# Kernel optimization log

Hardware: AMD Instinct MI355X
Metric: run time of the kernel (lower is better)

## Reference

```python
import jax, jax.numpy as jnp
import numpy as np

COMMITMENT_LOSS_WEIGHT = 0.25


def setup_inputs() -> dict:
    key = jax.random.key(0)
    k1, k2 = jax.random.split(key)
    B, H, W, C = 64, 32, 32, 256
    D, K = H * W, 1024  # embedding_dim = H*W per the rearrange+reshape in call()
    x = jax.random.normal(k1, (B, H, W, C), dtype=jnp.float32)
    # Orthogonal initializer (like tf.keras.initializers.Orthogonal) via QR
    E = jnp.linalg.qr(jax.random.normal(k2, (D, K), dtype=jnp.float32))[0]
    return {"x": x, "embeddings": E.astype(jnp.float32)}


def reference(x, embeddings):
    B, H, W, C = x.shape
    D = H * W  # embedding_dim
    # einops: 'b h w c -> b c (h w)'
    cont = jnp.transpose(x, (0, 3, 1, 2)).reshape(B, C, D)
    flat = cont.reshape(-1, D)  # [B*C, D]
    # squared L2 distances via norm + matmul (as in get_discretised)
    dists = (jnp.sum(flat * flat, axis=1, keepdims=True)
             + jnp.sum(embeddings * embeddings, axis=0)
             - 2.0 * (flat @ embeddings))  # [B*C, K]
    idx = jnp.argmin(dists, axis=1)  # [B*C]
    # one_hot @ embeddings.T == direct gather of codebook columns
    quantised = embeddings.T[idx].reshape(B, C, D)
    codebook_loss = jnp.mean((jax.lax.stop_gradient(cont) - quantised) ** 2)
    commitment_loss = COMMITMENT_LOSS_WEIGHT * jnp.mean(
        (cont - jax.lax.stop_gradient(quantised)) ** 2)
    loss = codebook_loss + commitment_loss  # layer add_loss terms, summed
    # einops: 'b c (h w) -> b h w c'
    q_bhwc = jnp.transpose(quantised.reshape(B, C, H, W), (0, 2, 3, 1))
    discretised = idx.reshape(-1, C)  # [B, C]
    # straight-through estimator
    q_out = x + jax.lax.stop_gradient(q_bhwc - x)
    return q_out, discretised, loss
```

## Files before the change

### kernel.cpp

```cpp
#include <hip/hip_runtime.h>
#include <float.h>
#include <stdint.h>

#define B_   64
#define C_   256
#define D_   1024
#define K_   1024
#define M_   16384
#define NX_  16777216
#define DISC_OFF NX_
#define LOSS_OFF (NX_ + M_)

typedef _Float16 h8 __attribute__((ext_vector_type(8)));
typedef float    f4 __attribute__((ext_vector_type(4)));

#define XSCALE 512.0f
#define ESCALE 2048.0f
#define DOT_UNSCALE_2 (2.0f / 1048576.0f)

#define WS_EH  0
#define WS_EL  524288
#define WS_CN  1048576
#define WS_PCN 1049600
#define WS_PV  1180672
#define WS_PI  1246208

__device__ __forceinline__ void async16(const _Float16* g, _Float16* l) {
    __builtin_amdgcn_global_load_lds(
        (const __attribute__((address_space(1))) unsigned int*)g,
        (__attribute__((address_space(3))) unsigned int*)l, 16, 0, 0);
}

__global__ __launch_bounds__(256) void esplit_kernel(const float* __restrict__ E,
                                                     _Float16* __restrict__ Eh,
                                                     _Float16* __restrict__ El,
                                                     float* __restrict__ pcn) {
    const int t  = threadIdx.x;
    const int o  = blockIdx.x;
    const int d0 = o * 8;
    const int n0 = t * 4;
    float4 row[8];
    #pragma unroll
    for (int i = 0; i < 8; ++i)
        row[i] = *(const float4*)(E + (size_t)(d0 + i) * K_ + n0);
    float s0 = 0.f, s1 = 0.f, s2 = 0.f, s3 = 0.f;
    h8 hh[4], ll[4];
    #pragma unroll
    for (int i = 0; i < 8; ++i) {
        const float* rp = (const float*)&row[i];
        #pragma unroll
        for (int j = 0; j < 4; ++j) {
            const float v  = rp[j];
            const float vs = v * ESCALE;
            const _Float16 h = (_Float16)vs;
            hh[j][i] = h;
            ll[j][i] = (_Float16)(vs - (float)h);
        }
        s0 = fmaf(rp[0], rp[0], s0);
        s1 = fmaf(rp[1], rp[1], s1);
        s2 = fmaf(rp[2], rp[2], s2);
        s3 = fmaf(rp[3], rp[3], s3);
    }
    float4 sv; sv.x = s0; sv.y = s1; sv.z = s2; sv.w = s3;
    *(float4*)(pcn + o * K_ + n0) = sv;
    const int nt    = n0 >> 4;
    const int kt    = o >> 2;
    const int lane0 = (n0 & 15) + (o & 3) * 16;
    const size_t base = ((size_t)(nt * 32 + kt) * 64 + lane0) * 8;
    #pragma unroll
    for (int j = 0; j < 4; ++j) {
        *(h8*)(Eh + base + (size_t)j * 8) = hh[j];
        *(h8*)(El + base + (size_t)j * 8) = ll[j];
    }
}

__global__ __launch_bounds__(256) void colnorm2_kernel(const float* __restrict__ pcn,
                                                       float* __restrict__ cn,
                                                       float* __restrict__ loss_slot) {
    __shared__ float sp[4][64];
    const int t    = threadIdx.x;
    const int col  = blockIdx.x * 64 + (t & 63);
    const int part = t >> 6;
    float s = 0.f;
    #pragma unroll 8
    for (int i = 0; i < 32; ++i) s += pcn[(part * 32 + i) * K_ + col];
    sp[part][t & 63] = s;
    __syncthreads();
    if (t < 64) cn[col] = (sp[0][t] + sp[1][t]) + (sp[2][t] + sp[3][t]);
    if (blockIdx.x == 0 && t == 0) *loss_slot = 0.0f;
}

__global__ __launch_bounds__(512, 2) void gemm_argmin_kernel(
        const float* __restrict__ x,
        const _Float16* __restrict__ Eh, const _Float16* __restrict__ El,
        const float* __restrict__ cn,
        float* __restrict__ pV, int* __restrict__ pI) {
    extern __shared__ _Float16 smem[];
    _Float16* Ab0 = smem;
    _Float16* Ab1 = smem + 8192;
    _Float16* Bb0 = smem + 16384;
    _Float16* Bb1 = smem + 32768;
    float* cV = (float*)(smem + 49152);
    int*   cI = (int*)(cV + 512);

    const int t    = threadIdx.x;
    const int rt   = blockIdx.x >> 2;
    const int ct   = blockIdx.x & 3;
    const int wave = t >> 6, lane = t & 63;
    const int lo16 = lane & 15, hi4 = lane >> 4;
    const int mq   = (wave & 1) * 64;
    const int nq   = (wave >> 1) * 64;
    const int nt0  = ct * 16;
    const int n0g  = ct * 256;

    const _Float16* srcB[4];
    _Float16* dstB0[4];
    _Float16* dstB1[4];
    #pragma unroll
    for (int i = 0; i < 4; ++i) {
        const int id = wave * 4 + i;
        const int plane = id >> 4, nt = id & 15;
        srcB[i]  = (plane ? El : Eh) + ((size_t)(nt0 + nt) * 32) * 512 + lane * 8;
        dstB0[i] = Bb0 + (plane * 16 + nt) * 512 + lane * 8;
        dstB1[i] = Bb1 + (plane * 16 + nt) * 512 + lane * 8;
    }

    const int b    = rt >> 1;
    const int c0   = (rt & 1) * 128;
    const int cl   = t & 127;
    const int ko8  = t >> 7;
    const float* xbase = x + ((size_t)(b * 1024 + ko8 * 8)) * 256 + c0 + cl;
    const int mt    = cl >> 4;
    const int lane0 = (cl & 15) + ko8 * 16;
    _Float16* wA[2] = { Ab0 + mt * 512 + lane0 * 8,
                        Ab1 + mt * 512 + lane0 * 8 };

    float av[8];
    auto loadA = [&](int s) {
        #pragma unroll
        for (int j = 0; j < 8; ++j)
            av[j] = xbase[((size_t)(s * 32) + j) * 256];
    };
    auto writeA = [&](_Float16* w) {
        h8 hh, ll;
        #pragma unroll
        for (int j = 0; j < 8; ++j) {
            const float vs = av[j] * XSCALE;
            const _Float16 h = (_Float16)vs;
            hh[j] = h;
            ll[j] = (_Float16)(vs - (float)h);
        }
        *(h8*)w = hh;
        *(h8*)(w + 4096) = ll;
    };

    f4 acc[4][4];
    const f4 zero = {0.f, 0.f, 0.f, 0.f};
    #pragma unroll
    for (int i = 0; i < 4; ++i)
        #pragma unroll
        for (int j = 0; j < 4; ++j) acc[i][j] = zero;

    #pragma unroll
    for (int i = 0; i < 4; ++i) async16(srcB[i], dstB0[i]);
    loadA(0);
    writeA(wA[0]);

    for (int s = 0; s < 32; ++s) {
        const int cur = s & 1;
        __syncthreads();
        if (s + 1 < 32) {
            #pragma unroll
            for (int i = 0; i < 4; ++i)
                async16(srcB[i] + (size_t)(s + 1) * 512, cur ? dstB0[i] : dstB1[i]);
            loadA(s + 1);
        }
        const _Float16* Abuf = cur ? Ab1 : Ab0;
        const _Float16* Bbuf = cur ? Bb1 : Bb0;

        h8 Bf[2][4];
        #pragma unroll
        for (int tn = 0; tn < 4; ++tn) {
            const int tixn = (nq >> 4) + tn;
            Bf[0][tn] = *(const h8*)&Bbuf[tixn * 512 + lane * 8];
            Bf[1][tn] = *(const h8*)&Bbuf[(16 + tixn) * 512 + lane * 8];
        }
        #pragma unroll
        for (int tm = 0; tm < 4; ++tm) {
            const int tixm = (mq >> 4) + tm;
            const h8 Ah = *(const h8*)&Abuf[tixm * 512 + lane * 8];
            const h8 Al = *(const h8*)&Abuf[(8 + tixm) * 512 + lane * 8];
            #pragma unroll
            for (int tn = 0; tn < 4; ++tn) {
                acc[tm][tn] = __builtin_amdgcn_mfma_f32_16x16x32_f16(Ah, Bf[0][tn], acc[tm][tn], 0, 0, 0);
                acc[tm][tn] = __builtin_amdgcn_mfma_f32_16x16x32_f16(Ah, Bf[1][tn], acc[tm][tn], 0, 0, 0);
                acc[tm][tn] = __builtin_amdgcn_mfma_f32_16x16x32_f16(Al, Bf[0][tn], acc[tm][tn], 0, 0, 0);
            }
        }
        if (s + 1 < 32) writeA(cur ? wA[0] : wA[1]);
    }

    float cnv[4];
    #pragma unroll
    for (int tn = 0; tn < 4; ++tn) cnv[tn] = cn[n0g + nq + tn * 16 + lo16];

    #pragma unroll
    for (int tm = 0; tm < 4; ++tm) {
        #pragma unroll
        for (int r = 0; r < 4; ++r) {
            float bv = FLT_MAX;
            int   bi = 0;
            #pragma unroll
            for (int tn = 0; tn < 4; ++tn) {
                const float v = cnv[tn] - acc[tm][tn][r] * DOT_UNSCALE_2;
                if (v < bv) { bv = v; bi = nq + tn * 16 + lo16; }
            }
            #pragma unroll
            for (int msk = 1; msk < 16; msk <<= 1) {
                const float ov = __shfl_xor(bv, msk, 64);
                const int   oi = __shfl_xor(bi, msk, 64);
                if (ov < bv || (ov == bv && oi < bi)) { bv = ov; bi = oi; }
            }
            if (lo16 == 0) {
                const int row = mq + tm * 16 + hi4 * 4 + r;
                const int g   = wave >> 1;
                cV[row * 4 + g] = bv;
                cI[row * 4 + g] = bi;
            }
        }
    }
    __syncthreads();
    if (t < 128) {
        float bv = FLT_MAX;
        int   bi = 0;
        #pragma unroll
        for (int g = 0; g < 4; ++g) {
            const float v = cV[t * 4 + g];
            const int   i = cI[t * 4 + g];
            if (v < bv || (v == bv && i < bi)) { bv = v; bi = i; }
        }
        const int row = rt * 128 + t;
        pV[row * 4 + ct] = bv;
        pI[row * 4 + ct] = n0g + bi;
    }
}

__global__ __launch_bounds__(256) void reduce_kernel(const float* __restrict__ pV,
                                                     const int* __restrict__ pI,
                                                     float* __restrict__ disc) {
    const int rid = blockIdx.x * 256 + threadIdx.x;
    float bv = FLT_MAX;
    int   bi = 0;
    #pragma unroll
    for (int c = 0; c < 4; ++c) {
        const float v = pV[rid * 4 + c];
        const int   i = pI[rid * 4 + c];
        if (v < bv || (v == bv && i < bi)) { bv = v; bi = i; }
    }
    disc[rid] = (float)bi;
}

__global__ __launch_bounds__(256) void finalize_kernel(const float* __restrict__ x,
                                                       const float* __restrict__ E,
                                                       const float* __restrict__ discf,
                                                       float* __restrict__ out,
                                                       float* __restrict__ loss) {
    __shared__ float Erow[1024];
    const int t = threadIdx.x;
    const int d = blockIdx.x;
    *(float4*)&Erow[t * 4] = *(const float4*)(E + (size_t)d * K_ + t * 4);
    __syncthreads();

    const int bl = t >> 6;
    const int c4 = (t & 63) * 4;
    float lsum = 0.f;
    #pragma unroll 4
    for (int bg = 0; bg < 64; bg += 4) {
        const int b = bg + bl;
        const float4 id4 = *(const float4*)(discf + b * 256 + c4);
        const size_t xoff = ((size_t)(b * 1024 + d) << 8) + c4;
        const float4 xv = *(const float4*)(x + xoff);
        const float e0 = Erow[(int)id4.x];
        const float e1 = Erow[(int)id4.y];
        const float e2 = Erow[(int)id4.z];
        const float e3 = Erow[(int)id4.w];
        float4 qv;
        qv.x = xv.x + (e0 - xv.x);
        qv.y = xv.y + (e1 - xv.y);
        qv.z = xv.z + (e2 - xv.z);
        qv.w = xv.w + (e3 - xv.w);
        *(float4*)(out + xoff) = qv;
        const float d0 = xv.x - e0, d1 = xv.y - e1, d2 = xv.z - e2, d3 = xv.w - e3;
        lsum += fmaf(d0, d0, fmaf(d1, d1, fmaf(d2, d2, d3 * d3)));
    }

    #pragma unroll
    for (int off = 32; off > 0; off >>= 1)
        lsum += __shfl_down(lsum, off);
    __shared__ float wsum[4];
    if ((t & 63) == 0) wsum[t >> 6] = lsum;
    __syncthreads();
    if (t == 0) {
        const float s = (wsum[0] + wsum[1]) + (wsum[2] + wsum[3]);
        atomicAdd(loss, s * (1.25f / 16777216.0f));
    }
}

extern "C" void kernel_launch(void* const* d_in, const int* in_sizes, int n_in,
                              void* d_out, int out_size, void* d_ws, size_t ws_size,
                              hipStream_t stream) {
    (void)in_sizes; (void)n_in; (void)out_size; (void)ws_size;
    const float* x = (const float*)d_in[0];
    const float* E = (const float*)d_in[1];
    float* out = (float*)d_out;
    float* ws  = (float*)d_ws;

    _Float16* Eh = (_Float16*)(ws + WS_EH);
    _Float16* El = (_Float16*)(ws + WS_EL);
    float* cn    = ws + WS_CN;
    float* pcn   = ws + WS_PCN;
    float* pV    = ws + WS_PV;
    int*   pI    = (int*)(ws + WS_PI);

    float* disc  = out + DISC_OFF;
    float* loss  = out + LOSS_OFF;

    hipFuncSetAttribute((const void*)gemm_argmin_kernel,
                        hipFuncAttributeMaxDynamicSharedMemorySize, 102400);

    esplit_kernel  <<<128,  256, 0, stream>>>(E, Eh, El, pcn);
    colnorm2_kernel<<<16,   256, 0, stream>>>(pcn, cn, loss);
    gemm_argmin_kernel<<<512, 512, 102400, stream>>>(x, Eh, El, cn, pV, pI);
    reduce_kernel  <<<64,   256, 0, stream>>>(pV, pI, disc);
    finalize_kernel<<<1024, 256, 0, stream>>>(x, E, disc, out, loss);
}
```

Before: 246.5 us.

## Stage x tiles into LDS asynchronously two steps ahead before fp16 split

```diff
diff --git a/kernel.cpp b/kernel.cpp
--- a/kernel.cpp
+++ b/kernel.cpp
@@ -26,6 +26,11 @@
 #define WS_PI  1246208
 
 __device__ __forceinline__ void async16(const _Float16* g, _Float16* l) {
+    __builtin_amdgcn_global_load_lds(
+        (const __attribute__((address_space(1))) unsigned int*)g,
+        (__attribute__((address_space(3))) unsigned int*)l, 16, 0, 0);
+}
+__device__ __forceinline__ void async16f(const float* g, float* l) {
     __builtin_amdgcn_global_load_lds(
         (const __attribute__((address_space(1))) unsigned int*)g,
         (__attribute__((address_space(3))) unsigned int*)l, 16, 0, 0);
@@ -96,12 +101,6 @@
         const float* __restrict__ cn,
         float* __restrict__ pV, int* __restrict__ pI) {
     extern __shared__ _Float16 smem[];
-    _Float16* Ab0 = smem;
-    _Float16* Ab1 = smem + 8192;
-    _Float16* Bb0 = smem + 16384;
-    _Float16* Bb1 = smem + 32768;
-    float* cV = (float*)(smem + 49152);
-    int*   cI = (int*)(cV + 512);
 
     const int t    = threadIdx.x;
     const int rt   = blockIdx.x >> 2;
@@ -114,44 +113,56 @@
     const int n0g  = ct * 256;
 
     const _Float16* srcB[4];
-    _Float16* dstB0[4];
-    _Float16* dstB1[4];
+    int offB[4];
     #pragma unroll
     for (int i = 0; i < 4; ++i) {
         const int id = wave * 4 + i;
         const int plane = id >> 4, nt = id & 15;
-        srcB[i]  = (plane ? El : Eh) + ((size_t)(nt0 + nt) * 32) * 512 + lane * 8;
-        dstB0[i] = Bb0 + (plane * 16 + nt) * 512 + lane * 8;
-        dstB1[i] = Bb1 + (plane * 16 + nt) * 512 + lane * 8;
-    }
-
-    const int b    = rt >> 1;
-    const int c0   = (rt & 1) * 128;
-    const int cl   = t & 127;
-    const int ko8  = t >> 7;
-    const float* xbase = x + ((size_t)(b * 1024 + ko8 * 8)) * 256 + c0 + cl;
-    const int mt    = cl >> 4;
+        srcB[i] = (plane ? El : Eh) + ((size_t)(nt0 + nt) * 32) * 512 + lane * 8;
+        offB[i] = (plane * 16 + nt) * 512 + lane * 8;
+    }
+    auto stageB = [&](int s) {
+        _Float16* bbuf = smem + (s & 1) * 16384;
+        #pragma unroll
+        for (int i = 0; i < 4; ++i)
+            async16(srcB[i] + (size_t)s * 512, bbuf + offB[i]);
+    };
+
+    const int b  = rt >> 1;
+    const int c0 = (rt & 1) * 128;
+    const float* xsrcA = x + ((size_t)(b * 1024 + (lane >> 5))) * 256 + c0 + (lane & 31) * 4;
+    const int cidA0 = wave * 2;
+    auto stageA = [&](int s) {
+        float* f32buf = (float*)(smem + 49152 + (s & 1) * 8192);
+        #pragma unroll
+        for (int i = 0; i < 2; ++i) {
+            const int cid = cidA0 + i;
+            async16f(xsrcA + (size_t)(s * 32 + cid * 2) * 256, f32buf + cid * 256 + lane * 4);
+        }
+    };
+
+    const int ko8   = wave >> 1;
+    const int cl    = (wave & 1) * 64 + lane;
+    const int mtl   = cl >> 4;
     const int lane0 = (cl & 15) + ko8 * 16;
-    _Float16* wA[2] = { Ab0 + mt * 512 + lane0 * 8,
-                        Ab1 + mt * 512 + lane0 * 8 };
-
-    float av[8];
-    auto loadA = [&](int s) {
-        #pragma unroll
-        for (int j = 0; j < 8; ++j)
-            av[j] = xbase[((size_t)(s * 32) + j) * 256];
-    };
-    auto writeA = [&](_Float16* w) {
+    const int fr    = ko8 * 8 * 128 + cl;
+    const int fw    = mtl * 512 + lane0 * 8;
+    auto convert = [&](int s) {
+        const float* f32buf = (const float*)(smem + 49152 + (s & 1) * 8192);
+        _Float16* fragbuf = smem + 32768 + (s & 1) * 8192;
+        float cv[8];
+        #pragma unroll
+        for (int j = 0; j < 8; ++j) cv[j] = f32buf[fr + j * 128];
         h8 hh, ll;
         #pragma unroll
         for (int j = 0; j < 8; ++j) {
-            const float vs = av[j] * XSCALE;
+            const float vs = cv[j] * XSCALE;
             const _Float16 h = (_Float16)vs;
             hh[j] = h;
             ll[j] = (_Float16)(vs - (float)h);
         }
-        *(h8*)w = hh;
-        *(h8*)(w + 4096) = ll;
+        *(h8*)(fragbuf + fw) = hh;
+        *(h8*)(fragbuf + 4096 + fw) = ll;
     };
 
     f4 acc[4][4];
@@ -161,23 +172,20 @@
         #pragma unroll
         for (int j = 0; j < 4; ++j) acc[i][j] = zero;
 
-    #pragma unroll
-    for (int i = 0; i < 4; ++i) async16(srcB[i], dstB0[i]);
-    loadA(0);
-    writeA(wA[0]);
+    stageA(0);
+    stageB(0);
+    __syncthreads();
+    convert(0);
+    stageA(1);
 
     for (int s = 0; s < 32; ++s) {
-        const int cur = s & 1;
         __syncthreads();
-        if (s + 1 < 32) {
-            #pragma unroll
-            for (int i = 0; i < 4; ++i)
-                async16(srcB[i] + (size_t)(s + 1) * 512, cur ? dstB0[i] : dstB1[i]);
-            loadA(s + 1);
-        }
-        const _Float16* Abuf = cur ? Ab1 : Ab0;
-        const _Float16* Bbuf = cur ? Bb1 : Bb0;
-
+        if (s + 2 < 32) stageA(s + 2);
+        if (s + 1 < 32) stageB(s + 1);
+        if (s + 1 < 32) convert(s + 1);
+
+        const _Float16* Abuf = smem + 32768 + (s & 1) * 8192;
+        const _Float16* Bbuf = smem + (s & 1) * 16384;
         h8 Bf[2][4];
         #pragma unroll
         for (int tn = 0; tn < 4; ++tn) {
@@ -189,7 +197,7 @@
         for (int tm = 0; tm < 4; ++tm) {
             const int tixm = (mq >> 4) + tm;
             const h8 Ah = *(const h8*)&Abuf[tixm * 512 + lane * 8];
-            const h8 Al = *(const h8*)&Abuf[(8 + tixm) * 512 + lane * 8];
+            const h8 Al = *(const h8*)&Abuf[4096 + tixm * 512 + lane * 8];
             #pragma unroll
             for (int tn = 0; tn < 4; ++tn) {
                 acc[tm][tn] = __builtin_amdgcn_mfma_f32_16x16x32_f16(Ah, Bf[0][tn], acc[tm][tn], 0, 0, 0);
@@ -197,8 +205,11 @@
                 acc[tm][tn] = __builtin_amdgcn_mfma_f32_16x16x32_f16(Al, Bf[0][tn], acc[tm][tn], 0, 0, 0);
             }
         }
-        if (s + 1 < 32) writeA(cur ? wA[0] : wA[1]);
-    }
+    }
+
+    __syncthreads();
+    float* cV = (float*)(smem + 49152);
+    int*   cI = (int*)(cV + 512);
 
     float cnv[4];
     #pragma unroll
@@ -325,12 +336,12 @@
     float* disc  = out + DISC_OFF;
     float* loss  = out + LOSS_OFF;
 
-    hipFuncSetAttribute((const void*)gemm_argmin_kernel,
-                        hipFuncAttributeMaxDynamicSharedMemorySize, 102400);
+    (void)hipFuncSetAttribute((const void*)gemm_argmin_kernel,
+                              hipFuncAttributeMaxDynamicSharedMemorySize, 131072);
 
     esplit_kernel  <<<128,  256, 0, stream>>>(E, Eh, El, pcn);
     colnorm2_kernel<<<16,   256, 0, stream>>>(pcn, cn, loss);
-    gemm_argmin_kernel<<<512, 512, 102400, stream>>>(x, Eh, El, cn, pV, pI);
+    gemm_argmin_kernel<<<512, 512, 131072, stream>>>(x, Eh, El, cn, pV, pI);
     reduce_kernel  <<<64,   256, 0, stream>>>(pV, pI, disc);
     finalize_kernel<<<1024, 256, 0, stream>>>(x, E, disc, out, loss);
 }
```

Result: no change. 243.9 us (-1.1%).
